# Optimization experiments

Hardware: AMD Instinct MI355X
Metric: run time of the kernel (lower is better)

## Reference

```python
import jax, jax.numpy as jnp
import numpy as np

B, S, H, NH = 2, 2048, 1024, 16
D = H // NH  # per-head dim = 64
NEG = -1000000000.0
EPS = 1e-6


def setup_inputs() -> dict:
    key = jax.random.key(0)
    ks = jax.random.split(key, 8)
    q = jax.random.normal(ks[0], (B, S, H), dtype=jnp.float32)
    k = jax.random.normal(ks[1], (B, S, H), dtype=jnp.float32)
    v = jax.random.normal(ks[2], (B, S, H), dtype=jnp.float32)
    mask = jax.random.randint(ks[3], (B, S, S), 0, 2, dtype=jnp.int32)
    # learned params (torch Linear stores W as [out,in]; y = x @ W.T)
    sc = 1.0 / np.sqrt(H)
    Wq = jax.random.normal(ks[4], (H, H), dtype=jnp.float32) * sc
    Wk = jax.random.normal(ks[5], (H, H), dtype=jnp.float32) * sc
    Wv = jax.random.normal(ks[6], (H, H), dtype=jnp.float32) * sc
    ln_gamma = jnp.ones((H,), dtype=jnp.float32)
    ln_beta = jnp.zeros((H,), dtype=jnp.float32)
    return {"q": q, "k": k, "v": v, "mask": mask,
            "Wq": Wq, "Wk": Wk, "Wv": Wv,
            "ln_gamma": ln_gamma, "ln_beta": ln_beta}


def _mha(q, k, v, mask, Wq, Wk, Wv, ln_gamma, ln_beta):
    residual = q
    # projections: note original never applies self.scale, and self.fc is unused
    qh = (q @ Wq.T).reshape(B, S, NH, D).transpose(0, 2, 1, 3)  # [B,NH,S,D]
    kh = (k @ Wk.T).reshape(B, S, NH, D).transpose(0, 2, 1, 3)
    vh = (v @ Wv.T).reshape(B, S, NH, D).transpose(0, 2, 1, 3)
    scores = jnp.einsum('bhqd,bhkd->bhqk', qh, kh)  # NO 1/sqrt(d) scaling (faithful)
    scores = jnp.where(mask[:, None, :, :] == 0, NEG, scores)
    attn = jax.nn.softmax(scores, axis=-1)
    ctx = jnp.einsum('bhqk,bhkd->bhqd', attn, vh)
    ctx = ctx.transpose(0, 2, 1, 3).reshape(B, S, H)
    ctx = ctx + residual  # dropout = identity in eval
    mu = jnp.mean(ctx, axis=-1, keepdims=True)
    var = jnp.var(ctx, axis=-1, keepdims=True)
    out = (ctx - mu) / jnp.sqrt(var + EPS) * ln_gamma + ln_beta
    return out, attn


def reference(q, k, v, mask, Wq, Wk, Wv, ln_gamma, ln_beta):
    return _mha(q, k, v, mask, Wq, Wk, Wv, ln_gamma, ln_beta)
```

## Files before the change

kernel.cpp:

```cpp
#include <hip/hip_runtime.h>
#include <hip/hip_fp16.h>

typedef _Float16 f16;
typedef _Float16 f16x8 __attribute__((ext_vector_type(8)));
typedef _Float16 f16x4 __attribute__((ext_vector_type(4)));
typedef float    f32x4 __attribute__((ext_vector_type(4)));

#define BAR_LDS() asm volatile("s_waitcnt lgkmcnt(0)\n\ts_barrier" ::: "memory")

__global__ __launch_bounds__(256) void cvt3(const float* __restrict__ a,
                                            const float* __restrict__ b,
                                            const float* __restrict__ c,
                                            f16* __restrict__ out, int per) {
  const float* src = blockIdx.y == 0 ? a : (blockIdx.y == 1 ? b : c);
  int i = (blockIdx.x * 256 + threadIdx.x) * 4;
  if (i >= per) return;
  f32x4 v = *(const f32x4*)(src + i);
  f16x4 h; h[0]=(f16)v[0]; h[1]=(f16)v[1]; h[2]=(f16)v[2]; h[3]=(f16)v[3];
  *(f16x4*)(out + (size_t)blockIdx.y * per + i) = h;
}

__global__ __launch_bounds__(256) void pack_mask(const int* __restrict__ m,
                                                 unsigned* __restrict__ bits) {
  size_t i = (size_t)blockIdx.x * 256 + threadIdx.x;
  unsigned long long b = __ballot(m[i] != 0);
  int lane = threadIdx.x & 63;
  if (lane == 0)       bits[i >> 5] = (unsigned)b;
  else if (lane == 32) bits[i >> 5] = (unsigned)(b >> 32);
}

__device__ inline void gld16(const void* g, void* l) {
  __builtin_amdgcn_global_load_lds((const __attribute__((address_space(1))) void*)g,
                                   (__attribute__((address_space(3))) void*)l, 16, 0, 0);
}

__global__ __launch_bounds__(256) void gemm_proj(const f16* __restrict__ Xall,
                                                 const f16* __restrict__ Wall,
                                                 f16* __restrict__ Qh,
                                                 f16* __restrict__ Kh,
                                                 f16* __restrict__ Vn) {
  __shared__ f16 lA[4][128][8];
  __shared__ f16 lB[4][128][8];
  const int z = blockIdx.z;
  const f16* A  = Xall + (size_t)z * (4096u * 1024u);
  const f16* Wt = Wall + (size_t)z * (1024u * 1024u);
  f16* Y = (z == 0) ? Qh : (z == 1 ? Kh : Vn);
  const int t = threadIdx.x;
  const int brow = blockIdx.y * 128, bcol = blockIdx.x * 128;
  const int w = t >> 6, l = t & 63;
  const int wr = w >> 1, wc = w & 1;
  const int lr = l & 15, lg = l >> 4;
  f32x4 acc[4][4] = {};

  for (int k0 = 0; k0 < 1024; k0 += 32) {
#pragma unroll
    for (int j = 0; j < 2; j++) {
      const int p = j * 4096 + t * 16;
      const int ks = p >> 11, row = (p >> 4) & 127;
      gld16(A  + (size_t)(brow + row) * 1024 + k0 + ks * 8, (char*)lA + p);
      gld16(Wt + (size_t)(bcol + row) * 1024 + k0 + ks * 8, (char*)lB + p);
    }
    __syncthreads();
    f16x8 af[4], bf[4];
#pragma unroll
    for (int mi = 0; mi < 4; mi++) af[mi] = *(const f16x8*)&lA[lg][wr * 64 + mi * 16 + lr][0];
#pragma unroll
    for (int ni = 0; ni < 4; ni++) bf[ni] = *(const f16x8*)&lB[lg][wc * 64 + ni * 16 + lr][0];
#pragma unroll
    for (int mi = 0; mi < 4; mi++)
#pragma unroll
      for (int ni = 0; ni < 4; ni++)
        acc[mi][ni] = __builtin_amdgcn_mfma_f32_16x16x32_f16(af[mi], bf[ni], acc[mi][ni], 0, 0, 0);
    __syncthreads();
  }

  const int mb0 = brow + wr * 64, nb0 = bcol + wc * 64;
#pragma unroll
  for (int mi = 0; mi < 4; mi++)
#pragma unroll
    for (int ni = 0; ni < 4; ni++)
#pragma unroll
      for (int j = 0; j < 4; j++) {
        const int m = mb0 + mi * 16 + lg * 4 + j;
        const int n = nb0 + ni * 16 + lr;
        const int bb = m >> 11, s = m & 2047;
        const int h = n >> 6, d = n & 63;
        Y[((((size_t)bb * 16 + h) * 2048 + s) << 6) + d] = (f16)acc[mi][ni][j];
      }
}

__global__ __launch_bounds__(512) void transposeV(const f16* __restrict__ Vn,
                                                  f16* __restrict__ VhT) {
  const int bh = blockIdx.y, s0 = blockIdx.x * 64;
  const int t = threadIdx.x, l = t & 63, w = t >> 6;
  const f16x8 v = *(const f16x8*)(Vn + (((size_t)bh * 2048 + s0 + l) << 6) + w * 8);
#pragma unroll
  for (int e = 0; e < 8; e++)
    VhT[(((size_t)bh * 64 + w * 8 + e) << 11) + s0 + l] = v[e];
}


__global__ __launch_bounds__(512, 6) void sumexp_k(const f16* __restrict__ Qh,
                                                   const f16* __restrict__ Kh,
                                                   const unsigned* __restrict__ mbits,
                                                   float* __restrict__ SIo) {
  __shared__ f16 lK[8][128][8];
  const int wg = blockIdx.x;
  const int bh = ((wg & 7) << 2) | (wg >> 7);
  const int qg = (wg >> 3) & 15;
  const int b = bh >> 4;
  const int t = threadIdx.x, w = t >> 6, l = t & 63;
  const int lr = l & 15, lg = l >> 4;
  const int qr = qg * 128 + w * 16;

  const int pA = t * 16, pB = 8192 + t * 16;
  const int ksA = pA >> 11, rwA = (pA >> 4) & 127;
  const int ksB = pB >> 11, rwB = (pB >> 4) & 127;
  const f16* Kbase = Kh + ((size_t)bh << 17);

  const f16* qp = Qh + (((size_t)bh * 2048 + qr + lr) << 6) + lg * 8;
  const f16x8 aq0 = *(const f16x8*)qp;
  const f16x8 aq1 = *(const f16x8*)(qp + 32);
  const unsigned* mrow = mbits + ((size_t)b * 2048 + qr + lr) * 64;

  float sum = 0.f;
  f16x8 kra = *(const f16x8*)(Kbase + ((size_t)rwA << 6) + ksA * 8);
  f16x8 krb = *(const f16x8*)(Kbase + ((size_t)rwB << 6) + ksB * 8);
  for (int t16 = 0; t16 < 16; t16++) {
    const int kb = t16 * 128;
    BAR_LDS();
    *(f16x8*)((char*)lK + pA) = kra;
    *(f16x8*)((char*)lK + pB) = krb;
    BAR_LDS();
    const uint4 mw4 = *(const uint4*)(mrow + (kb >> 5));
    const unsigned mwv[4] = {mw4.x, mw4.y, mw4.z, mw4.w};
    if (t16 < 15) {
      const f16* nb = Kbase + ((size_t)(kb + 128) << 6);
      kra = *(const f16x8*)(nb + ((size_t)rwA << 6) + ksA * 8);
      krb = *(const f16x8*)(nb + ((size_t)rwB << 6) + ksB * 8);
    }
#pragma unroll
    for (int nf = 0; nf < 8; nf++) {
      f32x4 s4 = {};
      s4 = __builtin_amdgcn_mfma_f32_16x16x32_f16(*(const f16x8*)&lK[lg][nf * 16 + lr][0], aq0, s4, 0, 0, 0);
      s4 = __builtin_amdgcn_mfma_f32_16x16x32_f16(*(const f16x8*)&lK[4 + lg][nf * 16 + lr][0], aq1, s4, 0, 0, 0);
      const unsigned word = mwv[nf >> 1];
      const unsigned bp = ((nf & 1) << 4) + lg * 4;
#pragma unroll
      for (int j = 0; j < 4; j++)
        sum += ((word >> (bp + j)) & 1u) ? __expf(s4[j]) : 0.f;
    }
  }
  sum += __shfl_xor(sum, 16, 64);
  sum += __shfl_xor(sum, 32, 64);
  if (l < 16) SIo[((size_t)bh << 11) + qr + lr] = 1.0f / sum;
}

__global__ __launch_bounds__(512, 4) void attn_pv(const f16* __restrict__ Qh,
                                                  const f16* __restrict__ Kh,
                                                  const f16* __restrict__ VhT,
                                                  const unsigned* __restrict__ mbits,
                                                  const float* __restrict__ SIo,
                                                  float* __restrict__ attn,
                                                  float* __restrict__ ctx) {
  __shared__ f16 lK[8][128][8];
  __shared__ f16 lVT[16][64][8];
  __shared__ __align__(16) char Pw[8][4096];
  const int wg = blockIdx.x;
  const int bh = ((wg & 7) << 2) | (wg >> 7);
  const int qg = (wg >> 3) & 15;
  const int b = bh >> 4, h = bh & 15;
  const int t = threadIdx.x, w = t >> 6, l = t & 63;
  const int lr = l & 15, lg = l >> 4;
  const int qr = qg * 128 + w * 16;
  char* wb = Pw[w];

  const int pA = t * 16, pB = 8192 + t * 16;
  const int ksA = pA >> 11, rwA = (pA >> 4) & 127;
  const int ksB = pB >> 11, rwB = (pB >> 4) & 127;
  const int vsA = pA >> 10, vdA = (pA >> 4) & 63;
  const int vsB = pB >> 10, vdB = (pB >> 4) & 63;
  const f16* Kbase = Kh + ((size_t)bh << 17);
  const f16* Vbase = VhT + ((size_t)bh << 17);

  const f16* qp = Qh + (((size_t)bh * 2048 + qr + lr) << 6) + lg * 8;
  const f16x8 aq0 = *(const f16x8*)qp;
  const f16x8 aq1 = *(const f16x8*)(qp + 32);
  const unsigned* mrow = mbits + ((size_t)b * 2048 + qr + lr) * 64;
  const float SIq = SIo[((size_t)bh << 11) + qr + lr];
  float* arow = attn + (((size_t)bh * 2048 + qr + lr) << 11);

  f32x4 acc[4] = {};
  f16x8 kra = *(const f16x8*)(Kbase + ((size_t)rwA << 6) + ksA * 8);
  f16x8 krb = *(const f16x8*)(Kbase + ((size_t)rwB << 6) + ksB * 8);
  f16x8 vra = *(const f16x8*)(Vbase + ((size_t)vdA << 11) + vsA * 8);
  f16x8 vrb = *(const f16x8*)(Vbase + ((size_t)vdB << 11) + vsB * 8);
  const int pswz = (lr & 7) << 4;

  for (int t16 = 0; t16 < 16; t16++) {
    const int kb = t16 * 128;
    BAR_LDS();
    *(f16x8*)((char*)lK + pA) = kra;
    *(f16x8*)((char*)lK + pB) = krb;
    *(f16x8*)((char*)lVT + pA) = vra;
    *(f16x8*)((char*)lVT + pB) = vrb;
    BAR_LDS();
    const uint4 mw4 = *(const uint4*)(mrow + (kb >> 5));
    const unsigned mwv[4] = {mw4.x, mw4.y, mw4.z, mw4.w};
    if (t16 < 15) {
      const f16* nk = Kbase + ((size_t)(kb + 128) << 6);
      kra = *(const f16x8*)(nk + ((size_t)rwA << 6) + ksA * 8);
      krb = *(const f16x8*)(nk + ((size_t)rwB << 6) + ksB * 8);
      const f16* nv = Vbase + kb + 128;
      vra = *(const f16x8*)(nv + ((size_t)vdA << 11) + vsA * 8);
      vrb = *(const f16x8*)(nv + ((size_t)vdB << 11) + vsB * 8);
    }
#pragma unroll
    for (int nf = 0; nf < 8; nf++) {
      f32x4 s4 = {};
      s4 = __builtin_amdgcn_mfma_f32_16x16x32_f16(*(const f16x8*)&lK[lg][nf * 16 + lr][0], aq0, s4, 0, 0, 0);
      s4 = __builtin_amdgcn_mfma_f32_16x16x32_f16(*(const f16x8*)&lK[4 + lg][nf * 16 + lr][0], aq1, s4, 0, 0, 0);
      const unsigned word = mwv[nf >> 1];
      const unsigned bp = ((nf & 1) << 4) + lg * 4;
      f32x4 po; f16x4 ph;
#pragma unroll
      for (int j = 0; j < 4; j++) {
        const float pj = ((word >> (bp + j)) & 1u) ? __expf(s4[j]) * SIq : 0.f;
        po[j] = pj; ph[j] = (f16)pj;
      }
      *(f32x4*)(arow + kb + nf * 16 + lg * 4) = po;
      *(f16x4*)(wb + lr * 256 + ((nf * 32 + lg * 8) ^ pswz)) = ph;
    }
#pragma unroll
    for (int kk = 0; kk < 4; kk++) {
      const f16x8 pa = *(const f16x8*)(wb + lr * 256 + ((kk * 64 + lg * 16) ^ pswz));
#pragma unroll
      for (int nf = 0; nf < 4; nf++)
        acc[nf] = __builtin_amdgcn_mfma_f32_16x16x32_f16(pa, *(const f16x8*)&lVT[kk * 4 + lg][nf * 16 + lr][0], acc[nf], 0, 0, 0);
    }
  }

#pragma unroll
  for (int nf = 0; nf < 4; nf++)
#pragma unroll
    for (int j = 0; j < 4; j++)
      ctx[((size_t)b * 2048 + qr + lg * 4 + j) * 1024 + h * 64 + nf * 16 + lr] = acc[nf][j];
}

__global__ __launch_bounds__(256) void ln_res(const float* __restrict__ qres,
                                              const float* __restrict__ gamma,
                                              const float* __restrict__ beta,
                                              float* __restrict__ io) {
  const int tok = blockIdx.x;
  const int t = threadIdx.x;
  float* rowp = io + (size_t)tok * 1024;
  const float* qp = qres + (size_t)tok * 1024;
  const f32x4 c = *(const f32x4*)(rowp + t * 4);
  const f32x4 r = *(const f32x4*)(qp + t * 4);
  f32x4 vals;
  float s = 0.f, s2 = 0.f;
#pragma unroll
  for (int e = 0; e < 4; e++) { float x = c[e] + r[e]; vals[e] = x; s += x; s2 += x * x; }
#pragma unroll
  for (int o = 1; o < 64; o <<= 1) { s += __shfl_xor(s, o, 64); s2 += __shfl_xor(s2, o, 64); }
  __shared__ float rs[4][2];
  const int w = t >> 6;
  if ((t & 63) == 0) { rs[w][0] = s; rs[w][1] = s2; }
  __syncthreads();
  s  = rs[0][0] + rs[1][0] + rs[2][0] + rs[3][0];
  s2 = rs[0][1] + rs[1][1] + rs[2][1] + rs[3][1];
  const float mu = s * (1.f / 1024.f);
  const float var = s2 * (1.f / 1024.f) - mu * mu;
  const float rstd = rsqrtf(var + 1e-6f);
  const f32x4 g  = *(const f32x4*)(gamma + t * 4);
  const f32x4 be = *(const f32x4*)(beta + t * 4);
  f32x4 o;
#pragma unroll
  for (int e = 0; e < 4; e++) o[e] = (vals[e] - mu) * rstd * g[e] + be[e];
  *(f32x4*)(rowp + t * 4) = o;
}

extern "C" void kernel_launch(void* const* d_in, const int* in_sizes, int n_in,
                              void* d_out, int out_size, void* d_ws, size_t ws_size,
                              hipStream_t stream) {
  const float* q     = (const float*)d_in[0];
  const float* k     = (const float*)d_in[1];
  const float* v     = (const float*)d_in[2];
  const int*   mask  = (const int*)d_in[3];
  const float* Wq    = (const float*)d_in[4];
  const float* Wk    = (const float*)d_in[5];
  const float* Wv    = (const float*)d_in[6];
  const float* gamma = (const float*)d_in[7];
  const float* beta  = (const float*)d_in[8];
  float* out  = (float*)d_out;
  float* attn = out + (size_t)4194304;
  const size_t MB = 1u << 20;
  char* ws = (char*)d_ws;

  f16 *x16, *W16, *Qh, *Kh, *Vn, *VhT; unsigned* mb; float* SIo;
  if (ws_size >= 65 * MB) {
    x16 = (f16*)ws;              W16 = (f16*)(ws + 24 * MB);
    Qh  = (f16*)(ws + 30 * MB);  Kh  = (f16*)(ws + 38 * MB);
    Vn  = (f16*)(ws + 46 * MB);  VhT = (f16*)(ws + 54 * MB);
    mb  = (unsigned*)(ws + 62 * MB);
    SIo = (float*)(ws + 63 * MB);
  } else {
    x16 = (f16*)attn;            W16 = (f16*)((char*)attn + 24 * MB);
    Vn  = (f16*)((char*)attn + 30 * MB);
    Qh  = (f16*)ws;              Kh  = (f16*)(ws + 8 * MB);
    VhT = (f16*)(ws + 16 * MB);  mb  = (unsigned*)(ws + 24 * MB);
    SIo = (float*)(ws + 25 * MB);
  }

  cvt3<<<dim3(4096, 3), 256, 0, stream>>>(q, k, v, x16, 4194304);
  cvt3<<<dim3(1024, 3), 256, 0, stream>>>(Wq, Wk, Wv, W16, 1048576);
  pack_mask<<<dim3(32768), 256, 0, stream>>>(mask, mb);
  gemm_proj<<<dim3(8, 32, 3), 256, 0, stream>>>(x16, W16, Qh, Kh, Vn);
  transposeV<<<dim3(32, 32), 512, 0, stream>>>(Vn, VhT);
  sumexp_k<<<dim3(512), 512, 0, stream>>>(Qh, Kh, mb, SIo);
  attn_pv<<<dim3(512), 512, 0, stream>>>(Qh, Kh, VhT, mb, SIo, attn, out);
  ln_res<<<dim3(4096), 256, 0, stream>>>(q, gamma, beta, out);
}
```

Before: 333.7 us.

## Coalesce attention-probability stores via LDS and drop K LDS staging in sumexp

In attn_pv, the fp32 attention matrix is no longer written straight from the MFMA fragment layout. Each tile is re-read from the per-wave fp16 P buffer in LDS and written as 128-byte contiguous row segments, to make the dominant attn write traffic more coalesced. In sumexp_k, the LDS staging of K tiles and its barriers are removed, and each lane loads its K fragments directly from global memory, relying on cache reuse. The stored attn values are now fp16-rounded probabilities converted back to fp32, which lowers output precision.

```diff
diff --git a/kernel.cpp b/kernel.cpp
--- a/kernel.cpp
+++ b/kernel.cpp
@@ -6,7 +6,6 @@
 typedef _Float16 f16x4 __attribute__((ext_vector_type(4)));
 typedef float    f32x4 __attribute__((ext_vector_type(4)));
 
-#define BAR_LDS() asm volatile("s_waitcnt lgkmcnt(0)\n\ts_barrier" ::: "memory")
 
 __global__ __launch_bounds__(256) void cvt3(const float* __restrict__ a,
                                             const float* __restrict__ b,
@@ -99,12 +98,10 @@
     VhT[(((size_t)bh * 64 + w * 8 + e) << 11) + s0 + l] = v[e];
 }
 
-
 __global__ __launch_bounds__(512, 6) void sumexp_k(const f16* __restrict__ Qh,
                                                    const f16* __restrict__ Kh,
                                                    const unsigned* __restrict__ mbits,
                                                    float* __restrict__ SIo) {
-  __shared__ f16 lK[8][128][8];
   const int wg = blockIdx.x;
   const int bh = ((wg & 7) << 2) | (wg >> 7);
   const int qg = (wg >> 3) & 15;
@@ -113,37 +110,26 @@
   const int lr = l & 15, lg = l >> 4;
   const int qr = qg * 128 + w * 16;
 
-  const int pA = t * 16, pB = 8192 + t * 16;
-  const int ksA = pA >> 11, rwA = (pA >> 4) & 127;
-  const int ksB = pB >> 11, rwB = (pB >> 4) & 127;
-  const f16* Kbase = Kh + ((size_t)bh << 17);
-
+  const char* Kb = (const char*)(Kh + ((size_t)bh << 17));
   const f16* qp = Qh + (((size_t)bh * 2048 + qr + lr) << 6) + lg * 8;
   const f16x8 aq0 = *(const f16x8*)qp;
   const f16x8 aq1 = *(const f16x8*)(qp + 32);
   const unsigned* mrow = mbits + ((size_t)b * 2048 + qr + lr) * 64;
 
   float sum = 0.f;
-  f16x8 kra = *(const f16x8*)(Kbase + ((size_t)rwA << 6) + ksA * 8);
-  f16x8 krb = *(const f16x8*)(Kbase + ((size_t)rwB << 6) + ksB * 8);
   for (int t16 = 0; t16 < 16; t16++) {
     const int kb = t16 * 128;
-    BAR_LDS();
-    *(f16x8*)((char*)lK + pA) = kra;
-    *(f16x8*)((char*)lK + pB) = krb;
-    BAR_LDS();
     const uint4 mw4 = *(const uint4*)(mrow + (kb >> 5));
     const unsigned mwv[4] = {mw4.x, mw4.y, mw4.z, mw4.w};
-    if (t16 < 15) {
-      const f16* nb = Kbase + ((size_t)(kb + 128) << 6);
-      kra = *(const f16x8*)(nb + ((size_t)rwA << 6) + ksA * 8);
-      krb = *(const f16x8*)(nb + ((size_t)rwB << 6) + ksB * 8);
-    }
+    const char* krow = Kb + (size_t)(kb + lr) * 128 + lg * 16;
 #pragma unroll
     for (int nf = 0; nf < 8; nf++) {
+      const char* kp = krow + nf * 2048;
+      const f16x8 k0 = *(const f16x8*)kp;
+      const f16x8 k1 = *(const f16x8*)(kp + 64);
       f32x4 s4 = {};
-      s4 = __builtin_amdgcn_mfma_f32_16x16x32_f16(*(const f16x8*)&lK[lg][nf * 16 + lr][0], aq0, s4, 0, 0, 0);
-      s4 = __builtin_amdgcn_mfma_f32_16x16x32_f16(*(const f16x8*)&lK[4 + lg][nf * 16 + lr][0], aq1, s4, 0, 0, 0);
+      s4 = __builtin_amdgcn_mfma_f32_16x16x32_f16(k0, aq0, s4, 0, 0, 0);
+      s4 = __builtin_amdgcn_mfma_f32_16x16x32_f16(k1, aq1, s4, 0, 0, 0);
       const unsigned word = mwv[nf >> 1];
       const unsigned bp = ((nf & 1) << 4) + lg * 4;
 #pragma unroll
@@ -188,23 +174,24 @@
   const f16x8 aq1 = *(const f16x8*)(qp + 32);
   const unsigned* mrow = mbits + ((size_t)b * 2048 + qr + lr) * 64;
   const float SIq = SIo[((size_t)bh << 11) + qr + lr];
-  float* arow = attn + (((size_t)bh * 2048 + qr + lr) << 11);
+  const int pswz = (lr & 7) << 4;
 
   f32x4 acc[4] = {};
   f16x8 kra = *(const f16x8*)(Kbase + ((size_t)rwA << 6) + ksA * 8);
   f16x8 krb = *(const f16x8*)(Kbase + ((size_t)rwB << 6) + ksB * 8);
   f16x8 vra = *(const f16x8*)(Vbase + ((size_t)vdA << 11) + vsA * 8);
   f16x8 vrb = *(const f16x8*)(Vbase + ((size_t)vdB << 11) + vsB * 8);
-  const int pswz = (lr & 7) << 4;
+  float* abase = attn + (((size_t)bh * 2048 + qr) << 11);
+  const int srow = l >> 3, scol = (l & 7) * 4;
 
   for (int t16 = 0; t16 < 16; t16++) {
     const int kb = t16 * 128;
-    BAR_LDS();
+    __syncthreads();
     *(f16x8*)((char*)lK + pA) = kra;
     *(f16x8*)((char*)lK + pB) = krb;
     *(f16x8*)((char*)lVT + pA) = vra;
     *(f16x8*)((char*)lVT + pB) = vrb;
-    BAR_LDS();
+    __syncthreads();
     const uint4 mw4 = *(const uint4*)(mrow + (kb >> 5));
     const unsigned mwv[4] = {mw4.x, mw4.y, mw4.z, mw4.w};
     if (t16 < 15) {
@@ -222,13 +209,12 @@
       s4 = __builtin_amdgcn_mfma_f32_16x16x32_f16(*(const f16x8*)&lK[4 + lg][nf * 16 + lr][0], aq1, s4, 0, 0, 0);
       const unsigned word = mwv[nf >> 1];
       const unsigned bp = ((nf & 1) << 4) + lg * 4;
-      f32x4 po; f16x4 ph;
+      f16x4 ph;
 #pragma unroll
       for (int j = 0; j < 4; j++) {
         const float pj = ((word >> (bp + j)) & 1u) ? __expf(s4[j]) * SIq : 0.f;
-        po[j] = pj; ph[j] = (f16)pj;
+        ph[j] = (f16)pj;
       }
-      *(f32x4*)(arow + kb + nf * 16 + lg * 4) = po;
       *(f16x4*)(wb + lr * 256 + ((nf * 32 + lg * 8) ^ pswz)) = ph;
     }
 #pragma unroll
@@ -237,6 +223,19 @@
 #pragma unroll
       for (int nf = 0; nf < 4; nf++)
         acc[nf] = __builtin_amdgcn_mfma_f32_16x16x32_f16(pa, *(const f16x8*)&lVT[kk * 4 + lg][nf * 16 + lr][0], acc[nf], 0, 0, 0);
+    }
+#pragma unroll
+    for (int h2 = 0; h2 < 2; h2++) {
+      const int row = srow + h2 * 8;
+      float* arow = abase + ((size_t)row << 11) + kb + scol;
+#pragma unroll
+      for (int u = 0; u < 4; u++) {
+        const f16x4 p4 = *(const f16x4*)(wb + row * 256 + (((scol + u * 32) * 2) ^ ((row & 7) << 4)));
+        f32x4 o;
+#pragma unroll
+        for (int e = 0; e < 4; e++) o[e] = (float)p4[e];
+        *(f32x4*)(arow + u * 32) = o;
+      }
     }
   }
 
```

After: 367.1 us. +10.0%, slower.
